# Performance work log

Hardware: AMD Instinct MI355X
Metric: run time of the kernel (lower is better)

## Reference

```python
import jax, jax.numpy as jnp
import numpy as np

N, D, E_EDGES = 50000, 128, 800000
HEADS, REL_DIM, N_RELS, LAYERS = 4, 64, 64, 2
HD = HEADS * D  # per-head out_channels == d_model (concat=False)
LN_EPS = 1e-5
NEG_SLOPE = 0.2


def setup_inputs() -> dict:
    key = jax.random.key(0)
    ks = jax.random.split(key, 12)
    s = 0.02
    return {
        "x_flat": jax.random.normal(ks[0], (N, D), jnp.float32),
        "edge_index": jax.random.randint(ks[1], (2, E_EDGES), 0, N, jnp.int32),
        "edge_type": jax.random.randint(ks[2], (E_EDGES,), 0, N_RELS, jnp.int32),
        "rel_emb": jax.random.normal(ks[3], (N_RELS, REL_DIM), jnp.float32) * s,
        # stacked params for LAYERS GATv2Conv layers
        "Wl": jax.random.normal(ks[4], (LAYERS, D, HD), jnp.float32) * s,
        "bl": jnp.zeros((LAYERS, HD), jnp.float32),
        "Wr": jax.random.normal(ks[5], (LAYERS, D, HD), jnp.float32) * s,
        "br": jnp.zeros((LAYERS, HD), jnp.float32),
        "We": jax.random.normal(ks[6], (LAYERS, REL_DIM, HD), jnp.float32) * s,
        "att": jax.random.normal(ks[7], (LAYERS, HEADS, D), jnp.float32) * s,
        "b_out": jnp.zeros((LAYERS, D), jnp.float32),
        "ln_g": jnp.ones((LAYERS, D), jnp.float32),
        "ln_b": jnp.zeros((LAYERS, D), jnp.float32),
    }


def _gatv2_layer(h, src, dst, eattr, Wl, bl, Wr, br, We, att, b_out):
    # h: [N, D] -> per-head transforms [N, H, C]
    xl = (h @ Wl + bl).reshape(N, HEADS, D)   # source transform (messages)
    xr = (h @ Wr + br).reshape(N, HEADS, D)   # target transform
    xe = (eattr @ We).reshape(-1, HEADS, D)   # edge transform (no bias, PyG)
    # GATv2 attention: a^T leaky_relu(xl_j + xr_i + xe)
    s = jax.nn.leaky_relu(xl[src] + xr[dst] + xe, NEG_SLOPE)  # [E, H, C]
    logits = jnp.einsum('ehc,hc->eh', s, att)                  # [E, H]
    # segment softmax over destination nodes
    mx = jax.ops.segment_max(logits, dst, num_segments=N)      # [N, H]
    ex = jnp.exp(logits - mx[dst])
    den = jax.ops.segment_sum(ex, dst, num_segments=N)
    alpha = ex / den[dst]                                      # [E, H]
    msg = xl[src] * alpha[..., None]                           # [E, H, C]
    out = jax.ops.segment_sum(msg.reshape(-1, HD), dst, num_segments=N)
    out = out.reshape(N, HEADS, D).mean(axis=1) + b_out        # concat=False -> mean
    return out


def _layernorm(x, g, b):
    mu = x.mean(-1, keepdims=True)
    var = ((x - mu) ** 2).mean(-1, keepdims=True)
    return (x - mu) * jax.lax.rsqrt(var + LN_EPS) * g + b


def reference(x_flat, edge_index, edge_type, rel_emb, Wl, bl, Wr, br, We, att, b_out, ln_g, ln_b):
    src, dst = edge_index[0], edge_index[1]
    eattr = rel_emb[edge_type]  # [E, REL_DIM]
    h = x_flat
    for l in range(LAYERS):
        m = _gatv2_layer(h, src, dst, eattr, Wl[l], bl[l], Wr[l], br[l], We[l], att[l], b_out[l])
        m = jax.nn.gelu(m, approximate=False)  # dropout in eval mode
        h = _layernorm(h + m, ln_g[l], ln_b[l])
    return h
```

## Files before the change

kernel.cpp:

```cpp
#include <hip/hip_runtime.h>
#include <hip/hip_bf16.h>

#define NN 50000
#define DM 128
#define EE 800000
#define NH 4
#define HDIM 512
#define NRELS 64
#define RDIM 64
#define LAYERS 2
#define NB 196

typedef short frag8 __attribute__((ext_vector_type(8)));
typedef float f32x4 __attribute__((ext_vector_type(4)));
typedef float f32x2 __attribute__((ext_vector_type(2)));

__device__ __forceinline__ float b2f(unsigned short u) {
    unsigned v = ((unsigned)u) << 16;
    union { unsigned u; float f; } c; c.u = v; return c.f;
}
__device__ __forceinline__ float b2f_lo(unsigned u) {
    union { unsigned u; float f; } c; c.u = u << 16; return c.f;
}
__device__ __forceinline__ float b2f_hi(unsigned u) {
    union { unsigned u; float f; } c; c.u = u & 0xFFFF0000u; return c.f;
}
__device__ __forceinline__ unsigned short f2b(float f) {
    union { float f; unsigned u; } c; c.f = f;
    unsigned u = c.u;
    u += 0x7FFFu + ((u >> 16) & 1u);
    return (unsigned short)(u >> 16);
}

__global__ void count_kernel(const int* __restrict__ dst, int* __restrict__ counts) {
    int e = blockIdx.x * 256 + threadIdx.x;
    if (e < EE) atomicAdd(&counts[dst[e]], 1);
}

__global__ __launch_bounds__(256) void psum_kernel(const int* __restrict__ counts,
                                                   int* __restrict__ psums) {
    int idx = blockIdx.x * 256 + threadIdx.x;
    int x = (idx < NN) ? counts[idx] : 0;
    int lane = threadIdx.x & 63, wv = threadIdx.x >> 6;
    #pragma unroll
    for (int d = 1; d < 64; d <<= 1) x += __shfl_xor(x, d, 64);
    __shared__ int ws[4];
    if (lane == 0) ws[wv] = x;
    __syncthreads();
    if (threadIdx.x == 0) psums[blockIdx.x] = ws[0] + ws[1] + ws[2] + ws[3];
}

__global__ __launch_bounds__(256) void pscan_kernel(const int* __restrict__ psums,
                                                    int* __restrict__ offs,
                                                    int* __restrict__ row_ptr) {
    int t = threadIdx.x;
    int x = (t < NB) ? psums[t] : 0;
    int lane = t & 63, wv = t >> 6;
    int incl = x;
    #pragma unroll
    for (int d = 1; d < 64; d <<= 1) {
        int y = __shfl_up(incl, d, 64);
        if (lane >= d) incl += y;
    }
    __shared__ int ws[4];
    if (lane == 63) ws[wv] = incl;
    __syncthreads();
    int off = 0;
    for (int k = 0; k < wv; ++k) off += ws[k];
    if (t < NB) offs[t] = incl + off - x;
    if (t == 0) row_ptr[0] = 0;
}

__global__ __launch_bounds__(256) void pfin_kernel(const int* __restrict__ counts,
                                                   const int* __restrict__ offs,
                                                   int* __restrict__ row_ptr,
                                                   int* __restrict__ cursor) {
    int idx = blockIdx.x * 256 + threadIdx.x;
    int x = (idx < NN) ? counts[idx] : 0;
    int lane = threadIdx.x & 63, wv = threadIdx.x >> 6;
    int incl = x;
    #pragma unroll
    for (int d = 1; d < 64; d <<= 1) {
        int y = __shfl_up(incl, d, 64);
        if (lane >= d) incl += y;
    }
    __shared__ int ws[4];
    if (lane == 63) ws[wv] = incl;
    __syncthreads();
    int off = offs[blockIdx.x];
    for (int k = 0; k < wv; ++k) off += ws[k];
    if (idx < NN) {
        int v = off + incl;
        row_ptr[idx + 1] = v;
        cursor[idx] = v - x;
    }
}

__global__ void scatter_kernel(const int* __restrict__ dst, int* __restrict__ cursor,
                               int* __restrict__ perm) {
    int e = blockIdx.x * 256 + threadIdx.x;
    if (e < EE) {
        int p = atomicAdd(&cursor[dst[e]], 1);
        perm[p] = e;
    }
}

__global__ void wconv_all_kernel(const float* __restrict__ Wl, const float* __restrict__ Wr,
                                 unsigned short* __restrict__ Wt) {
    int idx = blockIdx.x * 256 + threadIdx.x;
    if (idx >= 4 * DM * HDIM) return;
    int m = idx >> 16;
    int r = idx & 65535;
    int c = r >> 7, k = r & 127;
    int l = m >> 1;
    const float* W = (m & 1) ? Wr : Wl;
    Wt[idx] = f2b(W[(size_t)l * DM * HDIM + k * HDIM + c]);
}

__global__ void hb_kernel(const float* __restrict__ h, unsigned short* __restrict__ hb, int n4) {
    int idx = blockIdx.x * 256 + threadIdx.x;
    if (idx >= n4) return;
    float4 v = ((const float4*)h)[idx];
    ushort4 o;
    o.x = f2b(v.x); o.y = f2b(v.y); o.z = f2b(v.z); o.w = f2b(v.w);
    ((ushort4*)hb)[idx] = o;
}

__global__ void xe_kernel(const float* __restrict__ rel_emb,
                          const float* __restrict__ We,
                          float* __restrict__ xef) {
    int idx = blockIdx.x * 256 + threadIdx.x;
    if (idx >= LAYERS * NRELS * HDIM) return;
    int l  = idx / (NRELS * HDIM);
    int r  = (idx / HDIM) & (NRELS - 1);
    int hc = idx & (HDIM - 1);
    const float* Wel = We + (size_t)l * RDIM * HDIM;
    float s = 0.f;
    #pragma unroll 8
    for (int d = 0; d < RDIM; ++d) s += rel_emb[r * RDIM + d] * Wel[d * HDIM + hc];
    xef[idx] = s;
}

__global__ void be_kernel(const float* __restrict__ xef, const float* __restrict__ att,
                          float* __restrict__ be) {
    int tid = blockIdx.x * 256 + threadIdx.x;
    if (tid >= LAYERS * NRELS * NH) return;
    int l = tid >> 8;
    int r = (tid >> 2) & 63;
    int hh = tid & 3;
    const float* xp = xef + (size_t)l * NRELS * HDIM + r * HDIM + hh * DM;
    const float* ap = att + (size_t)l * HDIM + hh * DM;
    float s = 0.f;
    #pragma unroll 8
    for (int c = 0; c < DM; ++c) s += ap[c] * xp[c];
    be[tid] = 0.6f * s;
}

__global__ __launch_bounds__(256) void gemm_xlxr_ab_kernel(
    const unsigned short* __restrict__ hb,
    const unsigned short* __restrict__ WtL,
    const unsigned short* __restrict__ WtR,
    const float* __restrict__ bl, const float* __restrict__ br,
    const float* __restrict__ att_l,
    unsigned short* __restrict__ xl, unsigned short* __restrict__ xr,
    float* __restrict__ ab) {
    int w = threadIdx.x >> 6, lane = threadIdx.x & 63;
    int m0 = blockIdx.x * 32;
    int colL = lane & 15, kg = lane >> 4;

    frag8 a[2][4];
    #pragma unroll
    for (int mt = 0; mt < 2; ++mt) {
        int row = m0 + mt * 16 + colL;
        if (row >= NN) row = NN - 1;
        const unsigned short* arow = hb + (size_t)row * DM;
        #pragma unroll
        for (int kc = 0; kc < 4; ++kc) {
            uint4 raw = *(const uint4*)(arow + kc * 32 + kg * 8);
            a[mt][kc] = __builtin_bit_cast(frag8, raw);
        }
    }

    float prow[2][2][4];
    #pragma unroll
    for (int mt = 0; mt < 2; ++mt)
        #pragma unroll
        for (int mat = 0; mat < 2; ++mat)
            #pragma unroll
            for (int r = 0; r < 4; ++r) prow[mt][mat][r] = 0.f;

    #pragma unroll
    for (int mat = 0; mat < 2; ++mat) {
        const unsigned short* Wt = mat ? WtR : WtL;
        const float* bias = mat ? br : bl;
        unsigned short* out = mat ? xr : xl;
        #pragma unroll
        for (int nt = 0; nt < 8; ++nt) {
            int col = w * 128 + nt * 16 + colL;
            f32x4 acc0 = {0.f, 0.f, 0.f, 0.f};
            f32x4 acc1 = {0.f, 0.f, 0.f, 0.f};
            #pragma unroll
            for (int kc = 0; kc < 4; ++kc) {
                uint4 raw = *(const uint4*)(Wt + (size_t)col * DM + kc * 32 + kg * 8);
                frag8 b = __builtin_bit_cast(frag8, raw);
                acc0 = __builtin_amdgcn_mfma_f32_16x16x32_bf16(a[0][kc], b, acc0, 0, 0, 0);
                acc1 = __builtin_amdgcn_mfma_f32_16x16x32_bf16(a[1][kc], b, acc1, 0, 0, 0);
            }
            float bb = bias[col];
            float ac = att_l[col];
            #pragma unroll
            for (int r = 0; r < 4; ++r) {
                float v0 = acc0[r] + bb;
                float v1 = acc1[r] + bb;
                int row0 = m0 + kg * 4 + r;
                int row1 = row0 + 16;
                if (row0 < NN) out[(size_t)row0 * HDIM + col] = f2b(v0);
                if (row1 < NN) out[(size_t)row1 * HDIM + col] = f2b(v1);
                prow[0][mat][r] = fmaf(ac, v0, prow[0][mat][r]);
                prow[1][mat][r] = fmaf(ac, v1, prow[1][mat][r]);
            }
        }
    }
    #pragma unroll
    for (int d = 1; d < 16; d <<= 1) {
        #pragma unroll
        for (int mt = 0; mt < 2; ++mt)
            #pragma unroll
            for (int mat = 0; mat < 2; ++mat)
                #pragma unroll
                for (int r = 0; r < 4; ++r)
                    prow[mt][mat][r] += __shfl_xor(prow[mt][mat][r], d, 64);
    }
    if (colL == 0) {
        #pragma unroll
        for (int mt = 0; mt < 2; ++mt) {
            int row = m0 + mt * 16 + kg * 4;
            #pragma unroll
            for (int mat = 0; mat < 2; ++mat)
                #pragma unroll
                for (int r = 0; r < 4; ++r)
                    if (row + r < NN)
                        ab[(size_t)(row + r) * 8 + mat * 4 + w] = 0.6f * prow[mt][mat][r];
        }
    }
}

#define EDGE_LOAD(k, jj)                                              \
    uint2 oo##k = ox_l[jj];                                           \
    float cj##k = cl[jj][hh];                                         \
    uint4 vv##k = *(const uint4*)(xl_b + oo##k.x + l16);              \
    float4 e0##k = *(const float4*)(xe_b + oo##k.y + l32);            \
    float4 e1##k = *(const float4*)(xe_b + oo##k.y + l32 + 16);

#define EDGE_PROC(k) {                                                \
    f32x2 xp0 = f32x2{b2f_lo(vv##k.x), b2f_hi(vv##k.x)};              \
    f32x2 xp1 = f32x2{b2f_lo(vv##k.y), b2f_hi(vv##k.y)};              \
    f32x2 xp2 = f32x2{b2f_lo(vv##k.z), b2f_hi(vv##k.z)};              \
    f32x2 xp3 = f32x2{b2f_lo(vv##k.w), b2f_hi(vv##k.w)};              \
    f32x2 z0 = (xp0 + xrp0) + f32x2{e0##k.x, e0##k.y};                \
    f32x2 z1 = (xp1 + xrp1) + f32x2{e0##k.z, e0##k.w};                \
    f32x2 z2 = (xp2 + xrp2) + f32x2{e1##k.x, e1##k.y};                \
    f32x2 z3 = (xp3 + xrp3) + f32x2{e1##k.z, e1##k.w};                \
    float partial = fmaf(atv[0], fabsf(z0[0]),                        \
                    fmaf(atv[1], fabsf(z0[1]),                        \
                    fmaf(atv[2], fabsf(z1[0]),                        \
                    fmaf(atv[3], fabsf(z1[1]),                        \
                    fmaf(atv[4], fabsf(z2[0]),                        \
                    fmaf(atv[5], fabsf(z2[1]),                        \
                    fmaf(atv[6], fabsf(z3[0]), atv[7] * fabsf(z3[1])))))))); \
    _Pragma("unroll")                                                 \
    for (int d = 1; d < 16; d <<= 1) partial += __shfl_xor(partial, d, 64); \
    float we = __expf(partial + cj##k);                               \
    ss += we;                                                         \
    f32x2 wv = f32x2{we, we};                                         \
    acc0v += wv * xp0;                                                \
    acc1v += wv * xp1;                                                \
    acc2v += wv * xp2;                                                \
    acc3v += wv * xp3; }

__global__ __launch_bounds__(128) void node_fused_kernel(
    const int* __restrict__ row_ptr, const int* __restrict__ perm,
    const int* __restrict__ ei,
    const int* __restrict__ etype,
    const unsigned short* __restrict__ xl,
    const unsigned short* __restrict__ xr,
    const float* __restrict__ xef_l,
    const float* __restrict__ ab,
    const float* __restrict__ be_l,
    const float* __restrict__ att_l,
    const float* __restrict__ h_in,
    const float* __restrict__ b_out, const float* __restrict__ ln_g,
    const float* __restrict__ ln_b,
    float* __restrict__ h_out,
    unsigned short* __restrict__ hb_out) {
    int i = blockIdx.x;
    int t = threadIdx.x;
    int w = t >> 6, l = t & 63;
    int hh = l >> 4;
    __shared__ uint2 ox_l[128];
    __shared__ float cl[128][4];
    __shared__ float lsum[2][512];
    __shared__ float ssum_s[2][4];
    __shared__ float inv_s[4];
    __shared__ float red[4];

    int beg = row_ptr[i], end = row_ptr[i + 1];

    uint4 xrv = *(const uint4*)(xr + (size_t)i * HDIM + l * 8);
    f32x2 xrp0 = f32x2{b2f_lo(xrv.x), b2f_hi(xrv.x)};
    f32x2 xrp1 = f32x2{b2f_lo(xrv.y), b2f_hi(xrv.y)};
    f32x2 xrp2 = f32x2{b2f_lo(xrv.z), b2f_hi(xrv.z)};
    f32x2 xrp3 = f32x2{b2f_lo(xrv.w), b2f_hi(xrv.w)};
    float4 at0 = ((const float4*)(att_l + l * 8))[0];
    float4 at1 = ((const float4*)(att_l + l * 8))[1];
    float atv[8] = {at0.x * 0.4f, at0.y * 0.4f, at0.z * 0.4f, at0.w * 0.4f,
                    at1.x * 0.4f, at1.y * 0.4f, at1.z * 0.4f, at1.w * 0.4f};
    float4 bxv = ((const float4*)ab)[2 * i + 1];

    const char* xl_b = (const char*)xl;
    const char* xe_b = (const char*)xef_l;
    uint l16 = (uint)l << 4, l32 = (uint)l << 5;

    float ss = 0.f;
    f32x2 acc0v = f32x2{0.f, 0.f}, acc1v = f32x2{0.f, 0.f};
    f32x2 acc2v = f32x2{0.f, 0.f}, acc3v = f32x2{0.f, 0.f};

    for (int cb = beg; cb < end; cb += 128) {
        int mc = min(128, end - cb);
        if (t < mc) {
            int p = perm[cb + t];
            int s = ei[p];
            int r = etype[p];
            ox_l[t].x = (uint)s << 10;
            ox_l[t].y = (uint)r << 11;
            float4 a4  = ((const float4*)ab)[2 * s];
            float4 be4 = ((const float4*)be_l)[r];
            cl[t][0] = a4.x + bxv.x + be4.x;
            cl[t][1] = a4.y + bxv.y + be4.y;
            cl[t][2] = a4.z + bxv.z + be4.z;
            cl[t][3] = a4.w + bxv.w + be4.w;
        }
        __syncthreads();
        int half = mc >> 1;
        int jb = w ? half : 0;
        int je = w ? mc : half;
        int j = jb;
        for (; j + 4 <= je; j += 4) {
            EDGE_LOAD(0, j)
            EDGE_LOAD(1, j + 1)
            EDGE_LOAD(2, j + 2)
            EDGE_LOAD(3, j + 3)
            EDGE_PROC(0)
            EDGE_PROC(1)
            EDGE_PROC(2)
            EDGE_PROC(3)
        }
        for (; j < je; ++j) {
            EDGE_LOAD(0, j)
            EDGE_PROC(0)
        }
        __syncthreads();
    }

    float* lw = &lsum[w][l * 8];
    lw[0] = acc0v[0]; lw[1] = acc0v[1]; lw[2] = acc1v[0]; lw[3] = acc1v[1];
    lw[4] = acc2v[0]; lw[5] = acc2v[1]; lw[6] = acc3v[0]; lw[7] = acc3v[1];
    if ((l & 15) == 0) ssum_s[w][hh] = ss;
    __syncthreads();
    if (t < 4) {
        float s = ssum_s[0][t] + ssum_s[1][t];
        inv_s[t] = (s > 0.f) ? 1.f / s : 0.f;
    }
    __syncthreads();

    int c = t;
    float o = 0.f;
    #pragma unroll
    for (int h = 0; h < 4; ++h)
        o = fmaf(lsum[0][h * 128 + c] + lsum[1][h * 128 + c], inv_s[h], o);
    o = o * 0.25f + b_out[c];
    float ge = 0.5f * o * (1.f + erff(o * 0.70710678118654752f));
    float y = h_in[(size_t)i * DM + c] + ge;

    float a = y, b = y * y;
    int lane = t & 63, wid = t >> 6;
    #pragma unroll
    for (int d = 1; d < 64; d <<= 1) {
        a += __shfl_xor(a, d, 64);
        b += __shfl_xor(b, d, 64);
    }
    if (lane == 0) { red[wid * 2 + 0] = a; red[wid * 2 + 1] = b; }
    __syncthreads();
    float mean = (red[0] + red[2]) * (1.f / 128.f);
    float var = (red[1] + red[3]) * (1.f / 128.f) - mean * mean;
    float rs = rsqrtf(var + 1e-5f);
    float out = (y - mean) * rs * ln_g[c] + ln_b[c];
    h_out[(size_t)i * DM + c] = out;
    hb_out[(size_t)i * DM + c] = f2b(out);
}

extern "C" void kernel_launch(void* const* d_in, const int* in_sizes, int n_in,
                              void* d_out, int out_size, void* d_ws, size_t ws_size,
                              hipStream_t stream) {
    const float* x_flat   = (const float*)d_in[0];
    const int*   edge_idx = (const int*)d_in[1];
    const int*   edge_ty  = (const int*)d_in[2];
    const float* rel_emb  = (const float*)d_in[3];
    const float* Wl       = (const float*)d_in[4];
    const float* bl       = (const float*)d_in[5];
    const float* Wr       = (const float*)d_in[6];
    const float* br       = (const float*)d_in[7];
    const float* We       = (const float*)d_in[8];
    const float* att      = (const float*)d_in[9];
    const float* b_out    = (const float*)d_in[10];
    const float* ln_g     = (const float*)d_in[11];
    const float* ln_b     = (const float*)d_in[12];

    char* p = (char*)d_ws;
    auto carve = [&](size_t bytes) {
        void* r = (void*)p;
        p += (bytes + 255) & ~(size_t)255;
        return r;
    };
    unsigned short* xl     = (unsigned short*)carve((size_t)NN * HDIM * 2);
    unsigned short* xr     = (unsigned short*)carve((size_t)NN * HDIM * 2);
    float*          h1     = (float*)carve((size_t)NN * DM * 4);
    unsigned short* hb     = (unsigned short*)carve((size_t)NN * DM * 2);
    unsigned short* Wt     = (unsigned short*)carve((size_t)4 * DM * HDIM * 2);
    float*          xef    = (float*)carve((size_t)LAYERS * NRELS * HDIM * 4);
    float*          ab     = (float*)carve((size_t)NN * 8 * 4);
    float*          be     = (float*)carve((size_t)LAYERS * NRELS * NH * 4);
    int*            row_ptr= (int*)carve((size_t)(NN + 1) * 4);
    int*            counts = (int*)carve((size_t)NN * 4);
    int*            cursor = (int*)carve((size_t)NN * 4);
    int*            perm   = (int*)carve((size_t)EE * 4);
    int*            psums  = (int*)carve((size_t)NB * 4);
    int*            offs   = (int*)carve((size_t)NB * 4);

    const int* dst = edge_idx + EE;

    hipMemsetAsync(counts, 0, (size_t)NN * 4, stream);
    count_kernel<<<(EE + 255) / 256, 256, 0, stream>>>(dst, counts);
    psum_kernel<<<NB, 256, 0, stream>>>(counts, psums);
    pscan_kernel<<<1, 256, 0, stream>>>(psums, offs, row_ptr);
    pfin_kernel<<<NB, 256, 0, stream>>>(counts, offs, row_ptr, cursor);
    scatter_kernel<<<(EE + 255) / 256, 256, 0, stream>>>(dst, cursor, perm);

    wconv_all_kernel<<<(4 * DM * HDIM + 255) / 256, 256, 0, stream>>>(Wl, Wr, Wt);
    xe_kernel<<<(LAYERS * NRELS * HDIM + 255) / 256, 256, 0, stream>>>(rel_emb, We, xef);
    be_kernel<<<(LAYERS * NRELS * NH + 255) / 256, 256, 0, stream>>>(xef, att, be);
    hb_kernel<<<(NN * DM / 4 + 255) / 256, 256, 0, stream>>>(x_flat, hb, NN * DM / 4);

    const float* h_cur = x_flat;
    for (int l = 0; l < LAYERS; ++l) {
        float* h_next = (l == LAYERS - 1) ? (float*)d_out : h1;
        gemm_xlxr_ab_kernel<<<(NN + 31) / 32, 256, 0, stream>>>(
            hb,
            Wt + (size_t)(l * 2 + 0) * DM * HDIM,
            Wt + (size_t)(l * 2 + 1) * DM * HDIM,
            bl + (size_t)l * HDIM, br + (size_t)l * HDIM,
            att + (size_t)l * HDIM,
            xl, xr, ab);
        node_fused_kernel<<<NN, 128, 0, stream>>>(
            row_ptr, perm, edge_idx, edge_ty, xl, xr,
            xef + (size_t)l * NRELS * HDIM,
            ab, be + (size_t)l * NRELS * NH,
            att + (size_t)l * HDIM,
            h_cur,
            b_out + (size_t)l * DM, ln_g + (size_t)l * DM, ln_b + (size_t)l * DM,
            h_next, hb);
        h_cur = h_next;
    }
}
```

Before: 641.2 us.

## Map one wave per node, precompute per-edge logits, and store edge features in bf16

Restructures the node aggregation so each 64-lane wave handles one destination node, four nodes per block. This removes the cross-wave LDS reductions and block-wide syncs of the old two-wave-per-node scheme. A new edge_prep kernel gathers the source/relation logit terms and packs source and relation indices into a CSR-ordered stream, so the node kernel reads them contiguously instead of indirecting through perm. The relation edge-embedding table is now stored in bf16 to halve its gather bandwidth. The edge loop becomes a one-deep software prefetch instead of a 4-way unroll, which may expose more latency. The extra prep pass writes about 16 bytes per edge per layer.

```diff
diff --git a/kernel.cpp b/kernel.cpp
--- a/kernel.cpp
+++ b/kernel.cpp
@@ -128,7 +128,8 @@
 
 __global__ void xe_kernel(const float* __restrict__ rel_emb,
                           const float* __restrict__ We,
-                          float* __restrict__ xef) {
+                          float* __restrict__ xef,
+                          unsigned short* __restrict__ xeb) {
     int idx = blockIdx.x * 256 + threadIdx.x;
     if (idx >= LAYERS * NRELS * HDIM) return;
     int l  = idx / (NRELS * HDIM);
@@ -139,6 +140,7 @@
     #pragma unroll 8
     for (int d = 0; d < RDIM; ++d) s += rel_emb[r * RDIM + d] * Wel[d * HDIM + hc];
     xef[idx] = s;
+    xeb[idx] = f2b(s);
 }
 
 __global__ void be_kernel(const float* __restrict__ xef, const float* __restrict__ att,
@@ -156,6 +158,23 @@
     be[tid] = 0.6f * s;
 }
 
+__global__ void edge_prep_kernel(const int* __restrict__ perm, const int* __restrict__ ei,
+                                 const int* __restrict__ etype,
+                                 const float* __restrict__ ab, const float* __restrict__ be_l,
+                                 float* __restrict__ cle, unsigned* __restrict__ pkq) {
+    int q = blockIdx.x * 256 + threadIdx.x;
+    if (q >= EE) return;
+    int e = perm[q];
+    int s = ei[e];
+    int r = etype[e];
+    float4 a4 = ((const float4*)ab)[2 * s];
+    float4 b4 = ((const float4*)be_l)[r];
+    float4 o;
+    o.x = a4.x + b4.x; o.y = a4.y + b4.y; o.z = a4.z + b4.z; o.w = a4.w + b4.w;
+    ((float4*)cle)[q] = o;
+    pkq[q] = ((unsigned)s << 6) | (unsigned)r;
+}
+
 __global__ __launch_bounds__(256) void gemm_xlxr_ab_kernel(
     const unsigned short* __restrict__ hb,
     const unsigned short* __restrict__ WtL,
@@ -245,66 +264,27 @@
     }
 }
 
-#define EDGE_LOAD(k, jj)                                              \
-    uint2 oo##k = ox_l[jj];                                           \
-    float cj##k = cl[jj][hh];                                         \
-    uint4 vv##k = *(const uint4*)(xl_b + oo##k.x + l16);              \
-    float4 e0##k = *(const float4*)(xe_b + oo##k.y + l32);            \
-    float4 e1##k = *(const float4*)(xe_b + oo##k.y + l32 + 16);
-
-#define EDGE_PROC(k) {                                                \
-    f32x2 xp0 = f32x2{b2f_lo(vv##k.x), b2f_hi(vv##k.x)};              \
-    f32x2 xp1 = f32x2{b2f_lo(vv##k.y), b2f_hi(vv##k.y)};              \
-    f32x2 xp2 = f32x2{b2f_lo(vv##k.z), b2f_hi(vv##k.z)};              \
-    f32x2 xp3 = f32x2{b2f_lo(vv##k.w), b2f_hi(vv##k.w)};              \
-    f32x2 z0 = (xp0 + xrp0) + f32x2{e0##k.x, e0##k.y};                \
-    f32x2 z1 = (xp1 + xrp1) + f32x2{e0##k.z, e0##k.w};                \
-    f32x2 z2 = (xp2 + xrp2) + f32x2{e1##k.x, e1##k.y};                \
-    f32x2 z3 = (xp3 + xrp3) + f32x2{e1##k.z, e1##k.w};                \
-    float partial = fmaf(atv[0], fabsf(z0[0]),                        \
-                    fmaf(atv[1], fabsf(z0[1]),                        \
-                    fmaf(atv[2], fabsf(z1[0]),                        \
-                    fmaf(atv[3], fabsf(z1[1]),                        \
-                    fmaf(atv[4], fabsf(z2[0]),                        \
-                    fmaf(atv[5], fabsf(z2[1]),                        \
-                    fmaf(atv[6], fabsf(z3[0]), atv[7] * fabsf(z3[1])))))))); \
-    _Pragma("unroll")                                                 \
-    for (int d = 1; d < 16; d <<= 1) partial += __shfl_xor(partial, d, 64); \
-    float we = __expf(partial + cj##k);                               \
-    ss += we;                                                         \
-    f32x2 wv = f32x2{we, we};                                         \
-    acc0v += wv * xp0;                                                \
-    acc1v += wv * xp1;                                                \
-    acc2v += wv * xp2;                                                \
-    acc3v += wv * xp3; }
-
-__global__ __launch_bounds__(128) void node_fused_kernel(
-    const int* __restrict__ row_ptr, const int* __restrict__ perm,
-    const int* __restrict__ ei,
-    const int* __restrict__ etype,
+__global__ __launch_bounds__(256) void node_fused_kernel(
+    const int* __restrict__ row_ptr,
+    const float* __restrict__ cle,
+    const unsigned* __restrict__ pkq,
     const unsigned short* __restrict__ xl,
     const unsigned short* __restrict__ xr,
-    const float* __restrict__ xef_l,
+    const unsigned short* __restrict__ xeb_l,
     const float* __restrict__ ab,
-    const float* __restrict__ be_l,
     const float* __restrict__ att_l,
     const float* __restrict__ h_in,
     const float* __restrict__ b_out, const float* __restrict__ ln_g,
     const float* __restrict__ ln_b,
     float* __restrict__ h_out,
     unsigned short* __restrict__ hb_out) {
-    int i = blockIdx.x;
-    int t = threadIdx.x;
-    int w = t >> 6, l = t & 63;
+    int w = threadIdx.x >> 6, l = threadIdx.x & 63;
+    int i = blockIdx.x * 4 + w;
     int hh = l >> 4;
-    __shared__ uint2 ox_l[128];
-    __shared__ float cl[128][4];
-    __shared__ float lsum[2][512];
-    __shared__ float ssum_s[2][4];
-    __shared__ float inv_s[4];
-    __shared__ float red[4];
+    __shared__ float cl[4][64][4];
 
     int beg = row_ptr[i], end = row_ptr[i + 1];
+    int c0 = (l & 15) * 8;
 
     uint4 xrv = *(const uint4*)(xr + (size_t)i * HDIM + l * 8);
     f32x2 xrp0 = f32x2{b2f_lo(xrv.x), b2f_hi(xrv.x)};
@@ -316,87 +296,118 @@
     float atv[8] = {at0.x * 0.4f, at0.y * 0.4f, at0.z * 0.4f, at0.w * 0.4f,
                     at1.x * 0.4f, at1.y * 0.4f, at1.z * 0.4f, at1.w * 0.4f};
     float4 bxv = ((const float4*)ab)[2 * i + 1];
+    float4 hv0 = *(const float4*)(h_in + (size_t)i * DM + c0);
+    float4 hv1 = *(const float4*)(h_in + (size_t)i * DM + c0 + 4);
 
     const char* xl_b = (const char*)xl;
-    const char* xe_b = (const char*)xef_l;
-    uint l16 = (uint)l << 4, l32 = (uint)l << 5;
+    const char* xe_b = (const char*)xeb_l;
+    uint l16 = (uint)l << 4;
 
     float ss = 0.f;
-    f32x2 acc0v = f32x2{0.f, 0.f}, acc1v = f32x2{0.f, 0.f};
-    f32x2 acc2v = f32x2{0.f, 0.f}, acc3v = f32x2{0.f, 0.f};
-
-    for (int cb = beg; cb < end; cb += 128) {
-        int mc = min(128, end - cb);
-        if (t < mc) {
-            int p = perm[cb + t];
-            int s = ei[p];
-            int r = etype[p];
-            ox_l[t].x = (uint)s << 10;
-            ox_l[t].y = (uint)r << 11;
-            float4 a4  = ((const float4*)ab)[2 * s];
-            float4 be4 = ((const float4*)be_l)[r];
-            cl[t][0] = a4.x + bxv.x + be4.x;
-            cl[t][1] = a4.y + bxv.y + be4.y;
-            cl[t][2] = a4.z + bxv.z + be4.z;
-            cl[t][3] = a4.w + bxv.w + be4.w;
+    f32x2 acc0 = f32x2{0.f, 0.f}, acc1 = f32x2{0.f, 0.f};
+    f32x2 acc2 = f32x2{0.f, 0.f}, acc3 = f32x2{0.f, 0.f};
+
+    for (int cb = beg; cb < end; cb += 64) {
+        int mc = min(64, end - cb);
+        unsigned pkr = 0;
+        if (l < mc) {
+            float4 c4 = ((const float4*)cle)[cb + l];
+            pkr = pkq[cb + l];
+            cl[w][l][0] = c4.x + bxv.x;
+            cl[w][l][1] = c4.y + bxv.y;
+            cl[w][l][2] = c4.z + bxv.z;
+            cl[w][l][3] = c4.w + bxv.w;
         }
-        __syncthreads();
-        int half = mc >> 1;
-        int jb = w ? half : 0;
-        int je = w ? mc : half;
-        int j = jb;
-        for (; j + 4 <= je; j += 4) {
-            EDGE_LOAD(0, j)
-            EDGE_LOAD(1, j + 1)
-            EDGE_LOAD(2, j + 2)
-            EDGE_LOAD(3, j + 3)
-            EDGE_PROC(0)
-            EDGE_PROC(1)
-            EDGE_PROC(2)
-            EDGE_PROC(3)
+        unsigned pk0 = __shfl(pkr, 0, 64);
+        uint4 vvP = *(const uint4*)(xl_b + ((pk0 >> 6) << 10) + l16);
+        uint4 eeP = *(const uint4*)(xe_b + ((pk0 & 63u) << 10) + l16);
+        float cjP = cl[w][0][hh];
+        for (int j = 1; j <= mc; ++j) {
+            uint4 vv = vvP; uint4 ee = eeP; float cj = cjP;
+            if (j < mc) {
+                unsigned pkj = __shfl(pkr, j, 64);
+                vvP = *(const uint4*)(xl_b + ((pkj >> 6) << 10) + l16);
+                eeP = *(const uint4*)(xe_b + ((pkj & 63u) << 10) + l16);
+                cjP = cl[w][j][hh];
+            }
+            f32x2 xp0 = f32x2{b2f_lo(vv.x), b2f_hi(vv.x)};
+            f32x2 xp1 = f32x2{b2f_lo(vv.y), b2f_hi(vv.y)};
+            f32x2 xp2 = f32x2{b2f_lo(vv.z), b2f_hi(vv.z)};
+            f32x2 xp3 = f32x2{b2f_lo(vv.w), b2f_hi(vv.w)};
+            f32x2 z0 = (xp0 + xrp0) + f32x2{b2f_lo(ee.x), b2f_hi(ee.x)};
+            f32x2 z1 = (xp1 + xrp1) + f32x2{b2f_lo(ee.y), b2f_hi(ee.y)};
+            f32x2 z2 = (xp2 + xrp2) + f32x2{b2f_lo(ee.z), b2f_hi(ee.z)};
+            f32x2 z3 = (xp3 + xrp3) + f32x2{b2f_lo(ee.w), b2f_hi(ee.w)};
+            float partial = fmaf(atv[0], fabsf(z0[0]),
+                            fmaf(atv[1], fabsf(z0[1]),
+                            fmaf(atv[2], fabsf(z1[0]),
+                            fmaf(atv[3], fabsf(z1[1]),
+                            fmaf(atv[4], fabsf(z2[0]),
+                            fmaf(atv[5], fabsf(z2[1]),
+                            fmaf(atv[6], fabsf(z3[0]), atv[7] * fabsf(z3[1]))))))));
+            #pragma unroll
+            for (int d = 1; d < 16; d <<= 1) partial += __shfl_xor(partial, d, 64);
+            float we = __expf(partial + cj);
+            ss += we;
+            f32x2 wv = f32x2{we, we};
+            acc0 += wv * xp0;
+            acc1 += wv * xp1;
+            acc2 += wv * xp2;
+            acc3 += wv * xp3;
         }
-        for (; j < je; ++j) {
-            EDGE_LOAD(0, j)
-            EDGE_PROC(0)
-        }
-        __syncthreads();
-    }
-
-    float* lw = &lsum[w][l * 8];
-    lw[0] = acc0v[0]; lw[1] = acc0v[1]; lw[2] = acc1v[0]; lw[3] = acc1v[1];
-    lw[4] = acc2v[0]; lw[5] = acc2v[1]; lw[6] = acc3v[0]; lw[7] = acc3v[1];
-    if ((l & 15) == 0) ssum_s[w][hh] = ss;
-    __syncthreads();
-    if (t < 4) {
-        float s = ssum_s[0][t] + ssum_s[1][t];
-        inv_s[t] = (s > 0.f) ? 1.f / s : 0.f;
-    }
-    __syncthreads();
-
-    int c = t;
-    float o = 0.f;
-    #pragma unroll
-    for (int h = 0; h < 4; ++h)
-        o = fmaf(lsum[0][h * 128 + c] + lsum[1][h * 128 + c], inv_s[h], o);
-    o = o * 0.25f + b_out[c];
-    float ge = 0.5f * o * (1.f + erff(o * 0.70710678118654752f));
-    float y = h_in[(size_t)i * DM + c] + ge;
-
-    float a = y, b = y * y;
-    int lane = t & 63, wid = t >> 6;
-    #pragma unroll
-    for (int d = 1; d < 64; d <<= 1) {
-        a += __shfl_xor(a, d, 64);
-        b += __shfl_xor(b, d, 64);
-    }
-    if (lane == 0) { red[wid * 2 + 0] = a; red[wid * 2 + 1] = b; }
-    __syncthreads();
-    float mean = (red[0] + red[2]) * (1.f / 128.f);
-    float var = (red[1] + red[3]) * (1.f / 128.f) - mean * mean;
+    }
+
+    float invs = (ss > 0.f) ? 1.f / ss : 0.f;
+    float sv[8] = {acc0[0] * invs, acc0[1] * invs, acc1[0] * invs, acc1[1] * invs,
+                   acc2[0] * invs, acc2[1] * invs, acc3[0] * invs, acc3[1] * invs};
+    #pragma unroll
+    for (int d = 16; d < 64; d <<= 1)
+        #pragma unroll
+        for (int k = 0; k < 8; ++k) sv[k] += __shfl_xor(sv[k], d, 64);
+
+    float4 bo0 = *(const float4*)(b_out + c0);
+    float4 bo1 = *(const float4*)(b_out + c0 + 4);
+    float bov[8] = {bo0.x, bo0.y, bo0.z, bo0.w, bo1.x, bo1.y, bo1.z, bo1.w};
+    float hvv[8] = {hv0.x, hv0.y, hv0.z, hv0.w, hv1.x, hv1.y, hv1.z, hv1.w};
+    float yv[8];
+    float la = 0.f, lb = 0.f;
+    #pragma unroll
+    for (int k = 0; k < 8; ++k) {
+        float o = sv[k] * 0.25f + bov[k];
+        float ge = 0.5f * o * (1.f + erff(o * 0.70710678118654752f));
+        float y = hvv[k] + ge;
+        yv[k] = y; la += y; lb += y * y;
+    }
+    #pragma unroll
+    for (int d = 1; d < 16; d <<= 1) {
+        la += __shfl_xor(la, d, 64);
+        lb += __shfl_xor(lb, d, 64);
+    }
+    float mean = la * (1.f / 128.f);
+    float var = lb * (1.f / 128.f) - mean * mean;
     float rs = rsqrtf(var + 1e-5f);
-    float out = (y - mean) * rs * ln_g[c] + ln_b[c];
-    h_out[(size_t)i * DM + c] = out;
-    hb_out[(size_t)i * DM + c] = f2b(out);
+
+    if (l < 16) {
+        float4 g0 = *(const float4*)(ln_g + c0);
+        float4 g1 = *(const float4*)(ln_g + c0 + 4);
+        float4 q0 = *(const float4*)(ln_b + c0);
+        float4 q1 = *(const float4*)(ln_b + c0 + 4);
+        float gv[8] = {g0.x, g0.y, g0.z, g0.w, g1.x, g1.y, g1.z, g1.w};
+        float qv[8] = {q0.x, q0.y, q0.z, q0.w, q1.x, q1.y, q1.z, q1.w};
+        float ov[8];
+        #pragma unroll
+        for (int k = 0; k < 8; ++k)
+            ov[k] = (yv[k] - mean) * rs * gv[k] + qv[k];
+        float* hop = h_out + (size_t)i * DM + c0;
+        *(float4*)hop = make_float4(ov[0], ov[1], ov[2], ov[3]);
+        *(float4*)(hop + 4) = make_float4(ov[4], ov[5], ov[6], ov[7]);
+        uint4 ob;
+        ob.x = (unsigned)f2b(ov[0]) | ((unsigned)f2b(ov[1]) << 16);
+        ob.y = (unsigned)f2b(ov[2]) | ((unsigned)f2b(ov[3]) << 16);
+        ob.z = (unsigned)f2b(ov[4]) | ((unsigned)f2b(ov[5]) << 16);
+        ob.w = (unsigned)f2b(ov[6]) | ((unsigned)f2b(ov[7]) << 16);
+        *(uint4*)(hb_out + (size_t)i * DM + c0) = ob;
+    }
 }
 
 extern "C" void kernel_launch(void* const* d_in, const int* in_sizes, int n_in,
@@ -428,6 +439,7 @@
     unsigned short* hb     = (unsigned short*)carve((size_t)NN * DM * 2);
     unsigned short* Wt     = (unsigned short*)carve((size_t)4 * DM * HDIM * 2);
     float*          xef    = (float*)carve((size_t)LAYERS * NRELS * HDIM * 4);
+    unsigned short* xeb    = (unsigned short*)carve((size_t)LAYERS * NRELS * HDIM * 2);
     float*          ab     = (float*)carve((size_t)NN * 8 * 4);
     float*          be     = (float*)carve((size_t)LAYERS * NRELS * NH * 4);
     int*            row_ptr= (int*)carve((size_t)(NN + 1) * 4);
@@ -436,6 +448,8 @@
     int*            perm   = (int*)carve((size_t)EE * 4);
     int*            psums  = (int*)carve((size_t)NB * 4);
     int*            offs   = (int*)carve((size_t)NB * 4);
+    float*          cle    = (float*)carve((size_t)EE * 4 * 4);
+    unsigned*       pkq    = (unsigned*)carve((size_t)EE * 4);
 
     const int* dst = edge_idx + EE;
 
@@ -447,7 +461,7 @@
     scatter_kernel<<<(EE + 255) / 256, 256, 0, stream>>>(dst, cursor, perm);
 
     wconv_all_kernel<<<(4 * DM * HDIM + 255) / 256, 256, 0, stream>>>(Wl, Wr, Wt);
-    xe_kernel<<<(LAYERS * NRELS * HDIM + 255) / 256, 256, 0, stream>>>(rel_emb, We, xef);
+    xe_kernel<<<(LAYERS * NRELS * HDIM + 255) / 256, 256, 0, stream>>>(rel_emb, We, xef, xeb);
     be_kernel<<<(LAYERS * NRELS * NH + 255) / 256, 256, 0, stream>>>(xef, att, be);
     hb_kernel<<<(NN * DM / 4 + 255) / 256, 256, 0, stream>>>(x_flat, hb, NN * DM / 4);
 
@@ -461,10 +475,12 @@
             bl + (size_t)l * HDIM, br + (size_t)l * HDIM,
             att + (size_t)l * HDIM,
             xl, xr, ab);
-        node_fused_kernel<<<NN, 128, 0, stream>>>(
-            row_ptr, perm, edge_idx, edge_ty, xl, xr,
-            xef + (size_t)l * NRELS * HDIM,
-            ab, be + (size_t)l * NRELS * NH,
+        edge_prep_kernel<<<(EE + 255) / 256, 256, 0, stream>>>(
+            perm, edge_idx, edge_ty, ab, be + (size_t)l * NRELS * NH, cle, pkq);
+        node_fused_kernel<<<NN / 4, 256, 0, stream>>>(
+            row_ptr, cle, pkq, xl, xr,
+            xeb + (size_t)l * NRELS * HDIM,
+            ab,
             att + (size_t)l * HDIM,
             h_cur,
             b_out + (size_t)l * DM, ln_g + (size_t)l * DM, ln_b + (size_t)l * DM,
```

Result: faster. 627.0 us (-2.2%).
